# Kernel optimization log

Measured on AMD Instinct MI355X. Metric: run time of the kernel, lower is better.

The kernel has to match this reference:

```python
import jax, jax.numpy as jnp
import numpy as np

EMBED_DIM = 1024
NUM_HEADS = 16
HEAD_DIM = EMBED_DIM // NUM_HEADS


def setup_inputs() -> dict:
    key = jax.random.key(0)
    k1, k2, k3, k4, k5 = jax.random.split(key, 5)
    B, N, D = 2, 2048, EMBED_DIM
    s = 1.0 / np.sqrt(D)
    x = jax.random.normal(k1, (B, N, D), dtype=jnp.float32)
    qkv_w = jax.random.uniform(k2, (3 * D, D), minval=-s, maxval=s, dtype=jnp.float32)
    qkv_b = jax.random.uniform(k3, (3 * D,), minval=-s, maxval=s, dtype=jnp.float32)
    proj_w = jax.random.uniform(k4, (D, D), minval=-s, maxval=s, dtype=jnp.float32)
    proj_b = jax.random.uniform(k5, (D,), minval=-s, maxval=s, dtype=jnp.float32)
    return {"x": x, "qkv_w": qkv_w, "qkv_b": qkv_b, "proj_w": proj_w, "proj_b": proj_b}


def reference(x, qkv_w, qkv_b, proj_w, proj_b):
    B, N, D = x.shape
    H, Hd = NUM_HEADS, HEAD_DIM
    scale = Hd ** (-0.5)
    # QKV projection (torch Linear: x @ W.T + b)
    qkv = x @ qkv_w.T + qkv_b                      # [B, N, 3D]
    q, k, v = jnp.split(qkv, 3, axis=-1)
    def split_heads(t):
        return t.reshape(B, N, H, Hd).transpose(0, 2, 1, 3)  # [B, H, N, Hd]
    q, k, v = map(split_heads, (q, k, v))
    attn = jnp.einsum("bhqd,bhkd->bhqk", q, k) * scale       # [B, H, N, N]
    attn = jax.nn.softmax(attn, axis=-1)
    out = jnp.einsum("bhqk,bhkd->bhqd", attn, v)             # [B, H, N, Hd]
    out = out.transpose(0, 2, 1, 3).reshape(B, N, D)
    return out @ proj_w.T + proj_b
```

## Files before the change

kernel.cpp:

```cpp
#include <hip/hip_runtime.h>
#include <hip/hip_bf16.h>


#define DEV __device__ __forceinline__

typedef __attribute__((ext_vector_type(8))) __bf16 bf16x8;
typedef __attribute__((ext_vector_type(4))) float f32x4;

static DEV unsigned short f2bf(float f) {
  unsigned u = __builtin_bit_cast(unsigned, f);
  u += 0x7FFFu + ((u >> 16) & 1u);
  return (unsigned short)(u >> 16);
}

static DEV float fexp2(float x) {
#if __has_builtin(__builtin_amdgcn_exp2f)
  return __builtin_amdgcn_exp2f(x);
#else
  return __expf(x * 0.69314718055994531f);
#endif
}

static DEV float max3(float a, float b, float c) {
  return fmaxf(fmaxf(a, b), c);
}

static DEV void gld16(const void* g, void* l) {
  __builtin_amdgcn_global_load_lds(
      (const __attribute__((address_space(1))) unsigned int*)g,
      (__attribute__((address_space(3))) unsigned int*)l, 16, 0, 0);
}

static DEV f32x4 mfma16(bf16x8 a, bf16x8 b, f32x4 c) {
  return __builtin_amdgcn_mfma_f32_16x16x32_bf16(a, b, c, 0, 0, 0);
}

__global__ void k_conv(const float* __restrict__ x, const float* __restrict__ qw,
                       const float* __restrict__ pw, unsigned short* __restrict__ xb,
                       unsigned short* __restrict__ wqb, unsigned short* __restrict__ pwb) {
  int b = blockIdx.x;
  const float* s;
  unsigned short* d;
  int base;
  if (b < 4096)      { s = x;  d = xb;  base = b; }
  else if (b < 7168) { s = qw; d = wqb; base = b - 4096; }
  else               { s = pw; d = pwb; base = b - 7168; }
  int i = (base * 256 + threadIdx.x) * 4;
  float4 v = *reinterpret_cast<const float4*>(s + i);
  union { unsigned short h[4]; uint2 u; } cv;
  cv.h[0] = f2bf(v.x); cv.h[1] = f2bf(v.y); cv.h[2] = f2bf(v.z); cv.h[3] = f2bf(v.w);
  *reinterpret_cast<uint2*>(d + i) = cv.u;
}

__global__ __launch_bounds__(256) void k_qkv(
    const unsigned short* __restrict__ A, const unsigned short* __restrict__ W,
    const float* __restrict__ bias, unsigned short* __restrict__ Qb,
    unsigned short* __restrict__ Kb, unsigned short* __restrict__ Vt) {
  const int K = 1024;
  __shared__ __align__(16) unsigned short As[128 * 32], Bs[128 * 32];
  const int tid = threadIdx.x, lane = tid & 63, wid = tid >> 6;
  const int wm = wid >> 1, wn = wid & 1, fr = lane & 15, fg = lane >> 4;
  const size_t bm = blockIdx.x, bn = blockIdx.y;
  const unsigned short* gA = A + bm * 128 * K;
  const unsigned short* gW = W + bn * 128 * K;
  f32x4 acc[4][4] = {};
  for (int k0 = 0; k0 < K; k0 += 32) {
#pragma unroll
    for (int c = 0; c < 2; ++c) {
      int bi = c * 4096 + wid * 1024 + lane * 16;
      int row = bi >> 6, ce = (bi & 63) >> 1;
      gld16(gA + (size_t)row * K + k0 + ce, As + c * 2048 + wid * 512);
      gld16(gW + (size_t)row * K + k0 + ce, Bs + c * 2048 + wid * 512);
    }
    __syncthreads();
    bf16x8 af[4], bw[4];
#pragma unroll
    for (int m = 0; m < 4; ++m)
      af[m] = *reinterpret_cast<const bf16x8*>(As + (wm * 64 + m * 16 + fr) * 32 + fg * 8);
#pragma unroll
    for (int n = 0; n < 4; ++n)
      bw[n] = *reinterpret_cast<const bf16x8*>(Bs + (wn * 64 + n * 16 + fr) * 32 + fg * 8);
#pragma unroll
    for (int m = 0; m < 4; ++m)
#pragma unroll
      for (int n = 0; n < 4; ++n)
        acc[m][n] = mfma16(af[m], bw[n], acc[m][n]);
    __syncthreads();
  }
  const float QSCALE = 0.18033688011112043f;
  float bv[4];
#pragma unroll
  for (int n = 0; n < 4; ++n) bv[n] = bias[bn * 128 + wn * 64 + n * 16 + fr];
#pragma unroll
  for (int m = 0; m < 4; ++m)
#pragma unroll
    for (int n = 0; n < 4; ++n) {
      int f = (int)bn * 128 + wn * 64 + n * 16 + fr;
      int t = f >> 10, d = f & 1023, h = d >> 6, hd = d & 63;
      int token0 = (int)bm * 128 + wm * 64 + m * 16 + fg * 4;
      int b_ = token0 >> 11, nn0 = token0 & 2047;
      size_t bh = (size_t)(b_ * 16 + h);
      float v0 = acc[m][n][0] + bv[n], v1 = acc[m][n][1] + bv[n];
      float v2 = acc[m][n][2] + bv[n], v3 = acc[m][n][3] + bv[n];
      if (t == 0) {
        unsigned short* q = Qb + (bh * 2048 + nn0) * 64 + hd;
        q[0] = f2bf(v0 * QSCALE); q[64] = f2bf(v1 * QSCALE);
        q[128] = f2bf(v2 * QSCALE); q[192] = f2bf(v3 * QSCALE);
      } else if (t == 1) {
        unsigned short* k = Kb + (bh * 2048 + nn0) * 64 + hd;
        k[0] = f2bf(v0); k[64] = f2bf(v1); k[128] = f2bf(v2); k[192] = f2bf(v3);
      } else {
        union { unsigned short h[4]; uint2 u; } pk;
        pk.h[0] = f2bf(v0); pk.h[1] = f2bf(v1);
        pk.h[2] = f2bf(v2); pk.h[3] = f2bf(v3);
        *reinterpret_cast<uint2*>(Vt + (bh * 64 + hd) * 2048 + nn0) = pk.u;
      }
    }
}

static DEV void attn_tile(const unsigned short* __restrict__ Ksb,
                          const unsigned short* __restrict__ Vsb,
                          unsigned short* __restrict__ pw, const bf16x8* qf,
                          int fr, int fg, f32x4* accO, float& mrow, float& lpart) {
  f32x4 s[4] = {};
#pragma unroll
  for (int nf = 0; nf < 4; ++nf)
#pragma unroll
    for (int ks = 0; ks < 2; ++ks) {
      bf16x8 kf = *reinterpret_cast<const bf16x8*>(
          &Ksb[(nf * 16 + fr) * 64 + (((ks * 4 + fg) ^ (fr & 7)) * 8)]);
      s[nf] = mfma16(kf, qf[ks], s[nf]);
    }
  bf16x8 vf[2][4];
#pragma unroll
  for (int ks = 0; ks < 2; ++ks)
#pragma unroll
    for (int df = 0; df < 4; ++df)
      vf[ks][df] = *reinterpret_cast<const bf16x8*>(
          &Vsb[(df * 16 + fr) * 64 + (((ks * 4 + fg) ^ (fr & 7)) * 8)]);
  float m0 = max3(s[0][0], s[0][1], s[0][2]);
  float m1 = max3(s[0][3], s[1][0], s[1][1]);
  float m2 = max3(s[1][2], s[1][3], s[2][0]);
  float m3 = max3(s[2][1], s[2][2], s[2][3]);
  float m4 = max3(s[3][0], s[3][1], s[3][2]);
  float mymax = fmaxf(max3(m0, m1, m2), max3(m3, m4, s[3][3]));
  if (!__all(mymax <= mrow + 8.0f)) {
    float pmax = fmaxf(mymax, __shfl_xor(mymax, 16));
    pmax = fmaxf(pmax, __shfl_xor(pmax, 32));
    float mnew = fmaxf(mrow, pmax);
    float sc = fexp2(mrow - mnew);
    mrow = mnew;
    lpart *= sc;
    float scq[4];
#pragma unroll
    for (int r = 0; r < 4; ++r) scq[r] = __shfl(sc, fg * 4 + r);
#pragma unroll
    for (int df = 0; df < 4; ++df)
#pragma unroll
      for (int r = 0; r < 4; ++r) accO[df][r] *= scq[r];
  }
  float rs = 0.f;
#pragma unroll
  for (int nf = 0; nf < 4; ++nf) {
    union { unsigned short h[4]; uint2 u; } pk;
#pragma unroll
    for (int r = 0; r < 4; ++r) {
      float p = fexp2(s[nf][r] - mrow);
      pk.h[r] = f2bf(p);
      rs += p;
    }
    *reinterpret_cast<uint2*>(
        &pw[fr * 64 + (((2 * nf + (fg >> 1)) ^ (fr & 7)) * 8) + (fg & 1) * 4]) = pk.u;
  }
  lpart += rs;
  bf16x8 pf[2];
#pragma unroll
  for (int ks = 0; ks < 2; ++ks)
    pf[ks] = *reinterpret_cast<const bf16x8*>(
        &pw[fr * 64 + (((ks * 4 + fg) ^ (fr & 7)) * 8)]);
#pragma unroll
  for (int df = 0; df < 4; ++df)
#pragma unroll
    for (int ks = 0; ks < 2; ++ks)
      accO[df] = mfma16(pf[ks], vf[ks][df], accO[df]);
}

__global__ __launch_bounds__(256) void k_attn(
    const unsigned short* __restrict__ Qb, const unsigned short* __restrict__ Kb,
    const unsigned short* __restrict__ Vt, unsigned short* __restrict__ Ob) {
  __shared__ __align__(16) unsigned short Ks0[64 * 64], Ks1[64 * 64];
  __shared__ __align__(16) unsigned short Vs0[64 * 64], Vs1[64 * 64];
  __shared__ __align__(16) unsigned short p_lds[4][16 * 64];
  const int tid = threadIdx.x, lane = tid & 63, w = tid >> 6;
  const int fr = lane & 15, fg = lane >> 4;
  const int bid = (int)(blockIdx.x & 7) * 128 + (int)(blockIdx.x >> 3);
  const int qt = bid & 31, bh = bid >> 5;
  const unsigned short* Qp = Qb + ((size_t)bh * 2048 + qt * 64 + w * 16) * 64;
  const unsigned short* Kp = Kb + (size_t)bh * 2048 * 64;
  const unsigned short* Vp = Vt + (size_t)bh * 64 * 2048;
  unsigned short* pw = &p_lds[w][0];

  const int crow0 = w * 16 + (lane >> 3);
  bf16x8 qf[2];
#pragma unroll
  for (int ks = 0; ks < 2; ++ks)
    qf[ks] = *reinterpret_cast<const bf16x8*>(Qp + fr * 64 + ks * 32 + fg * 8);

  f32x4 accO[4] = {};
  float mrow = -1e30f, lpart = 0.f;

#define STAGE(KDST, VDST, kti)                                                \
  {                                                                           \
    const unsigned short* Kt_ = Kp + (kti) * 64 * 64;                         \
    _Pragma("unroll")                                                         \
    for (int j = 0; j < 2; ++j) {                                             \
      int cr = crow0 + j * 8;                                                 \
      int cs = (lane & 7) ^ (cr & 7);                                         \
      gld16(Kt_ + cr * 64 + cs * 8, (KDST) + (w * 2 + j) * 512);              \
      gld16(Vp + (size_t)cr * 2048 + (kti) * 64 + cs * 8,                     \
            (VDST) + (w * 2 + j) * 512);                                      \
    }                                                                         \
  }

  STAGE(Ks0, Vs0, 0);
  STAGE(Ks1, Vs1, 1);
  __syncthreads();
  for (int i = 0; i < 16; ++i) {
    attn_tile(Ks0, Vs0, pw, qf, fr, fg, accO, mrow, lpart);
    __syncthreads();
    if (i < 15) STAGE(Ks0, Vs0, 2 * i + 2);
    attn_tile(Ks1, Vs1, pw, qf, fr, fg, accO, mrow, lpart);
    __syncthreads();
    if (i < 15) STAGE(Ks1, Vs1, 2 * i + 3);
  }
#undef STAGE
  float lrow = lpart;
  lrow += __shfl_xor(lrow, 16);
  lrow += __shfl_xor(lrow, 32);
  float linv = 1.f / lrow;
  float lq[4];
#pragma unroll
  for (int r = 0; r < 4; ++r) lq[r] = __shfl(linv, fg * 4 + r);
  const int b_ = bh >> 4, h = bh & 15;
#pragma unroll
  for (int df = 0; df < 4; ++df)
#pragma unroll
    for (int r = 0; r < 4; ++r) {
      int nn = qt * 64 + w * 16 + fg * 4 + r;
      int d = df * 16 + fr;
      Ob[(size_t)(b_ * 2048 + nn) * 1024 + h * 64 + d] = f2bf(accO[df][r] * lq[r]);
    }
}

__global__ __launch_bounds__(256) void k_proj(
    const unsigned short* __restrict__ A, const unsigned short* __restrict__ W,
    const float* __restrict__ bias, float* __restrict__ out) {
  const int K = 1024;
  __shared__ __align__(16) unsigned short As[128 * 32], Bs[128 * 32];
  const int tid = threadIdx.x, lane = tid & 63, wid = tid >> 6;
  const int wm = wid >> 1, wn = wid & 1, fr = lane & 15, fg = lane >> 4;
  const size_t bm = blockIdx.x, bn = blockIdx.y;
  const unsigned short* gA = A + bm * 128 * K;
  const unsigned short* gW = W + bn * 128 * K;
  f32x4 acc[4][4] = {};
  for (int k0 = 0; k0 < K; k0 += 32) {
#pragma unroll
    for (int c = 0; c < 2; ++c) {
      int bi = c * 4096 + wid * 1024 + lane * 16;
      int row = bi >> 6, ce = (bi & 63) >> 1;
      gld16(gA + (size_t)row * K + k0 + ce, As + c * 2048 + wid * 512);
      gld16(gW + (size_t)row * K + k0 + ce, Bs + c * 2048 + wid * 512);
    }
    __syncthreads();
    bf16x8 af[4], bw[4];
#pragma unroll
    for (int m = 0; m < 4; ++m)
      af[m] = *reinterpret_cast<const bf16x8*>(As + (wm * 64 + m * 16 + fr) * 32 + fg * 8);
#pragma unroll
    for (int n = 0; n < 4; ++n)
      bw[n] = *reinterpret_cast<const bf16x8*>(Bs + (wn * 64 + n * 16 + fr) * 32 + fg * 8);
#pragma unroll
    for (int m = 0; m < 4; ++m)
#pragma unroll
      for (int n = 0; n < 4; ++n)
        acc[m][n] = mfma16(af[m], bw[n], acc[m][n]);
    __syncthreads();
  }
  float bv[4];
#pragma unroll
  for (int n = 0; n < 4; ++n) bv[n] = bias[bn * 128 + wn * 64 + n * 16 + fr];
#pragma unroll
  for (int m = 0; m < 4; ++m)
#pragma unroll
    for (int n = 0; n < 4; ++n)
#pragma unroll
      for (int r = 0; r < 4; ++r) {
        size_t token = bm * 128 + wm * 64 + m * 16 + fg * 4 + r;
        int f = (int)bn * 128 + wn * 64 + n * 16 + fr;
        out[token * 1024 + f] = acc[m][n][r] + bv[n];
      }
}

extern "C" void kernel_launch(void* const* d_in, const int* in_sizes, int n_in,
                              void* d_out, int out_size, void* d_ws, size_t ws_size,
                              hipStream_t stream) {
  const float* x      = (const float*)d_in[0];
  const float* qkv_w  = (const float*)d_in[1];
  const float* qkv_b  = (const float*)d_in[2];
  const float* proj_w = (const float*)d_in[3];
  const float* proj_b = (const float*)d_in[4];
  float* out = (float*)d_out;
  char* ws = (char*)d_ws;
  unsigned short* xb  = (unsigned short*)(ws);
  unsigned short* wqb = (unsigned short*)(ws + (size_t)(8u << 20));
  unsigned short* pwb = (unsigned short*)(ws + (size_t)(14u << 20));
  unsigned short* Qb  = (unsigned short*)(ws + (size_t)(16u << 20));
  unsigned short* Kb  = (unsigned short*)(ws + (size_t)(24u << 20));
  unsigned short* Vt  = (unsigned short*)(ws + (size_t)(32u << 20));
  unsigned short* Ob  = (unsigned short*)(ws + (size_t)(40u << 20));

  k_conv<<<8192, 256, 0, stream>>>(x, qkv_w, proj_w, xb, wqb, pwb);
  k_qkv<<<dim3(32, 24), 256, 0, stream>>>(xb, wqb, qkv_b, Qb, Kb, Vt);
  k_attn<<<1024, 256, 0, stream>>>(Qb, Kb, Vt, Ob);
  k_proj<<<dim3(32, 8), 256, 0, stream>>>(Ob, pwb, proj_b, out);
}
```

Measured before the change: 206.2 us.

## Double-buffer GEMM LDS tiles and tune attention tile scheduling priorities

The QKV and projection GEMMs now use two LDS buffers, prefetching the next K-slice while MFMAs run on the current one. This removes one barrier per step and hides global-load latency, at the cost of twice the LDS per block, which may lower occupancy. In the attention kernel, swizzled LDS column offsets are precomputed once per thread, and s_setprio raises wave priority around the MFMA blocks. The softmax row-sum is also restructured into a tree reduction.

```diff
diff --git a/kernel.cpp b/kernel.cpp
--- a/kernel.cpp
+++ b/kernel.cpp
@@ -52,39 +52,54 @@
   *reinterpret_cast<uint2*>(d + i) = cv.u;
 }
 
+static DEV void gemm_tile(const unsigned short* __restrict__ Asb,
+                          const unsigned short* __restrict__ Bsb,
+                          int wm, int wn, int fr, int fg, f32x4 (&acc)[4][4]) {
+  bf16x8 af[4], bw[4];
+#pragma unroll
+  for (int m = 0; m < 4; ++m)
+    af[m] = *reinterpret_cast<const bf16x8*>(Asb + (wm * 64 + m * 16 + fr) * 32 + fg * 8);
+#pragma unroll
+  for (int n = 0; n < 4; ++n)
+    bw[n] = *reinterpret_cast<const bf16x8*>(Bsb + (wn * 64 + n * 16 + fr) * 32 + fg * 8);
+#pragma unroll
+  for (int m = 0; m < 4; ++m)
+#pragma unroll
+    for (int n = 0; n < 4; ++n)
+      acc[m][n] = mfma16(af[m], bw[n], acc[m][n]);
+}
+
+#define QSTAGE(ab, k0)                                                        \
+  {                                                                           \
+    _Pragma("unroll")                                                         \
+    for (int c = 0; c < 2; ++c) {                                             \
+      int bi = c * 4096 + wid * 1024 + lane * 16;                             \
+      int row = bi >> 6, ce = (bi & 63) >> 1;                                 \
+      gld16(gA + (size_t)row * K + (k0) + ce, &As[ab][c * 2048 + wid * 512]); \
+      gld16(gW + (size_t)row * K + (k0) + ce, &Bs[ab][c * 2048 + wid * 512]); \
+    }                                                                         \
+  }
+
 __global__ __launch_bounds__(256) void k_qkv(
     const unsigned short* __restrict__ A, const unsigned short* __restrict__ W,
     const float* __restrict__ bias, unsigned short* __restrict__ Qb,
     unsigned short* __restrict__ Kb, unsigned short* __restrict__ Vt) {
   const int K = 1024;
-  __shared__ __align__(16) unsigned short As[128 * 32], Bs[128 * 32];
+  __shared__ __align__(16) unsigned short As[2][128 * 32], Bs[2][128 * 32];
   const int tid = threadIdx.x, lane = tid & 63, wid = tid >> 6;
   const int wm = wid >> 1, wn = wid & 1, fr = lane & 15, fg = lane >> 4;
   const size_t bm = blockIdx.x, bn = blockIdx.y;
   const unsigned short* gA = A + bm * 128 * K;
   const unsigned short* gW = W + bn * 128 * K;
   f32x4 acc[4][4] = {};
-  for (int k0 = 0; k0 < K; k0 += 32) {
-#pragma unroll
-    for (int c = 0; c < 2; ++c) {
-      int bi = c * 4096 + wid * 1024 + lane * 16;
-      int row = bi >> 6, ce = (bi & 63) >> 1;
-      gld16(gA + (size_t)row * K + k0 + ce, As + c * 2048 + wid * 512);
-      gld16(gW + (size_t)row * K + k0 + ce, Bs + c * 2048 + wid * 512);
-    }
-    __syncthreads();
-    bf16x8 af[4], bw[4];
-#pragma unroll
-    for (int m = 0; m < 4; ++m)
-      af[m] = *reinterpret_cast<const bf16x8*>(As + (wm * 64 + m * 16 + fr) * 32 + fg * 8);
-#pragma unroll
-    for (int n = 0; n < 4; ++n)
-      bw[n] = *reinterpret_cast<const bf16x8*>(Bs + (wn * 64 + n * 16 + fr) * 32 + fg * 8);
-#pragma unroll
-    for (int m = 0; m < 4; ++m)
-#pragma unroll
-      for (int n = 0; n < 4; ++n)
-        acc[m][n] = mfma16(af[m], bw[n], acc[m][n]);
+  QSTAGE(0, 0);
+  __syncthreads();
+  for (int i = 0; i < 16; ++i) {
+    QSTAGE(1, i * 64 + 32);
+    gemm_tile(As[0], Bs[0], wm, wn, fr, fg, acc);
+    __syncthreads();
+    if (i < 15) QSTAGE(0, i * 64 + 64);
+    gemm_tile(As[1], Bs[1], wm, wn, fr, fg, acc);
     __syncthreads();
   }
   const float QSCALE = 0.18033688011112043f;
@@ -121,23 +136,25 @@
 static DEV void attn_tile(const unsigned short* __restrict__ Ksb,
                           const unsigned short* __restrict__ Vsb,
                           unsigned short* __restrict__ pw, const bf16x8* qf,
-                          int fr, int fg, f32x4* accO, float& mrow, float& lpart) {
+                          int fr, int fg, const int* kcol, const int* pcol,
+                          f32x4* accO, float& mrow, float& lpart) {
+  const int prow = fr * 64;
   f32x4 s[4] = {};
+  __builtin_amdgcn_s_setprio(1);
 #pragma unroll
   for (int nf = 0; nf < 4; ++nf)
 #pragma unroll
     for (int ks = 0; ks < 2; ++ks) {
-      bf16x8 kf = *reinterpret_cast<const bf16x8*>(
-          &Ksb[(nf * 16 + fr) * 64 + (((ks * 4 + fg) ^ (fr & 7)) * 8)]);
+      bf16x8 kf = *reinterpret_cast<const bf16x8*>(&Ksb[(nf * 16 + fr) * 64 + kcol[ks]]);
       s[nf] = mfma16(kf, qf[ks], s[nf]);
     }
+  __builtin_amdgcn_s_setprio(0);
   bf16x8 vf[2][4];
 #pragma unroll
   for (int ks = 0; ks < 2; ++ks)
 #pragma unroll
     for (int df = 0; df < 4; ++df)
-      vf[ks][df] = *reinterpret_cast<const bf16x8*>(
-          &Vsb[(df * 16 + fr) * 64 + (((ks * 4 + fg) ^ (fr & 7)) * 8)]);
+      vf[ks][df] = *reinterpret_cast<const bf16x8*>(&Vsb[(df * 16 + fr) * 64 + kcol[ks]]);
   float m0 = max3(s[0][0], s[0][1], s[0][2]);
   float m1 = max3(s[0][3], s[1][0], s[1][1]);
   float m2 = max3(s[1][2], s[1][3], s[2][0]);
@@ -159,30 +176,28 @@
 #pragma unroll
       for (int r = 0; r < 4; ++r) accO[df][r] *= scq[r];
   }
-  float rs = 0.f;
+  float rsn[4];
 #pragma unroll
   for (int nf = 0; nf < 4; ++nf) {
+    float p0 = fexp2(s[nf][0] - mrow), p1 = fexp2(s[nf][1] - mrow);
+    float p2 = fexp2(s[nf][2] - mrow), p3 = fexp2(s[nf][3] - mrow);
     union { unsigned short h[4]; uint2 u; } pk;
-#pragma unroll
-    for (int r = 0; r < 4; ++r) {
-      float p = fexp2(s[nf][r] - mrow);
-      pk.h[r] = f2bf(p);
-      rs += p;
-    }
-    *reinterpret_cast<uint2*>(
-        &pw[fr * 64 + (((2 * nf + (fg >> 1)) ^ (fr & 7)) * 8) + (fg & 1) * 4]) = pk.u;
-  }
-  lpart += rs;
+    pk.h[0] = f2bf(p0); pk.h[1] = f2bf(p1); pk.h[2] = f2bf(p2); pk.h[3] = f2bf(p3);
+    rsn[nf] = (p0 + p1) + (p2 + p3);
+    *reinterpret_cast<uint2*>(&pw[prow + pcol[nf]]) = pk.u;
+  }
+  lpart += (rsn[0] + rsn[1]) + (rsn[2] + rsn[3]);
   bf16x8 pf[2];
 #pragma unroll
   for (int ks = 0; ks < 2; ++ks)
-    pf[ks] = *reinterpret_cast<const bf16x8*>(
-        &pw[fr * 64 + (((ks * 4 + fg) ^ (fr & 7)) * 8)]);
+    pf[ks] = *reinterpret_cast<const bf16x8*>(&pw[prow + kcol[ks]]);
+  __builtin_amdgcn_s_setprio(1);
 #pragma unroll
   for (int df = 0; df < 4; ++df)
 #pragma unroll
     for (int ks = 0; ks < 2; ++ks)
       accO[df] = mfma16(pf[ks], vf[ks][df], accO[df]);
+  __builtin_amdgcn_s_setprio(0);
 }
 
 __global__ __launch_bounds__(256) void k_attn(
@@ -200,6 +215,13 @@
   const unsigned short* Vp = Vt + (size_t)bh * 64 * 2048;
   unsigned short* pw = &p_lds[w][0];
 
+  int kcol[2], pcol[4];
+#pragma unroll
+  for (int ks = 0; ks < 2; ++ks) kcol[ks] = ((ks * 4 + fg) ^ (fr & 7)) * 8;
+#pragma unroll
+  for (int nf = 0; nf < 4; ++nf)
+    pcol[nf] = (((2 * nf + (fg >> 1)) ^ (fr & 7)) * 8) + (fg & 1) * 4;
+
   const int crow0 = w * 16 + (lane >> 3);
   bf16x8 qf[2];
 #pragma unroll
@@ -226,10 +248,10 @@
   STAGE(Ks1, Vs1, 1);
   __syncthreads();
   for (int i = 0; i < 16; ++i) {
-    attn_tile(Ks0, Vs0, pw, qf, fr, fg, accO, mrow, lpart);
+    attn_tile(Ks0, Vs0, pw, qf, fr, fg, kcol, pcol, accO, mrow, lpart);
     __syncthreads();
     if (i < 15) STAGE(Ks0, Vs0, 2 * i + 2);
-    attn_tile(Ks1, Vs1, pw, qf, fr, fg, accO, mrow, lpart);
+    attn_tile(Ks1, Vs1, pw, qf, fr, fg, kcol, pcol, accO, mrow, lpart);
     __syncthreads();
     if (i < 15) STAGE(Ks1, Vs1, 2 * i + 3);
   }
@@ -256,34 +278,21 @@
     const unsigned short* __restrict__ A, const unsigned short* __restrict__ W,
     const float* __restrict__ bias, float* __restrict__ out) {
   const int K = 1024;
-  __shared__ __align__(16) unsigned short As[128 * 32], Bs[128 * 32];
+  __shared__ __align__(16) unsigned short As[2][128 * 32], Bs[2][128 * 32];
   const int tid = threadIdx.x, lane = tid & 63, wid = tid >> 6;
   const int wm = wid >> 1, wn = wid & 1, fr = lane & 15, fg = lane >> 4;
   const size_t bm = blockIdx.x, bn = blockIdx.y;
   const unsigned short* gA = A + bm * 128 * K;
   const unsigned short* gW = W + bn * 128 * K;
   f32x4 acc[4][4] = {};
-  for (int k0 = 0; k0 < K; k0 += 32) {
-#pragma unroll
-    for (int c = 0; c < 2; ++c) {
-      int bi = c * 4096 + wid * 1024 + lane * 16;
-      int row = bi >> 6, ce = (bi & 63) >> 1;
-      gld16(gA + (size_t)row * K + k0 + ce, As + c * 2048 + wid * 512);
-      gld16(gW + (size_t)row * K + k0 + ce, Bs + c * 2048 + wid * 512);
-    }
-    __syncthreads();
-    bf16x8 af[4], bw[4];
-#pragma unroll
-    for (int m = 0; m < 4; ++m)
-      af[m] = *reinterpret_cast<const bf16x8*>(As + (wm * 64 + m * 16 + fr) * 32 + fg * 8);
-#pragma unroll
-    for (int n = 0; n < 4; ++n)
-      bw[n] = *reinterpret_cast<const bf16x8*>(Bs + (wn * 64 + n * 16 + fr) * 32 + fg * 8);
-#pragma unroll
-    for (int m = 0; m < 4; ++m)
-#pragma unroll
-      for (int n = 0; n < 4; ++n)
-        acc[m][n] = mfma16(af[m], bw[n], acc[m][n]);
+  QSTAGE(0, 0);
+  __syncthreads();
+  for (int i = 0; i < 16; ++i) {
+    QSTAGE(1, i * 64 + 32);
+    gemm_tile(As[0], Bs[0], wm, wn, fr, fg, acc);
+    __syncthreads();
+    if (i < 15) QSTAGE(0, i * 64 + 64);
+    gemm_tile(As[1], Bs[1], wm, wn, fr, fg, acc);
     __syncthreads();
   }
   float bv[4];
```

After: 217.2 us. 5.3% more time.
